# Optimization experiments

Measured on AMD Instinct MI355X. Metric: run time of the kernel, lower is better.

The kernel has to match this reference:

```python
import jax, jax.numpy as jnp
import numpy as np

N = 50000        # number of nodes (A is [N, N] sparse adjacency)
NNZ = 1600000    # number of edges (avg degree 32)
UNITS = 64       # output feature dim


def setup_inputs() -> dict:
    key = jax.random.key(0)
    k1, k2, k3, k4 = jax.random.split(key, 4)
    rows = jax.random.randint(k1, (NNZ,), 0, N, dtype=jnp.int32)
    cols = jax.random.randint(k2, (NNZ,), 0, N, dtype=jnp.int32)
    values = jax.random.uniform(k3, (NNZ,), dtype=jnp.float32)
    # glorot-like scale for kernel of shape (N, UNITS)
    kernel = jax.random.normal(k4, (N, UNITS), dtype=jnp.float32) * np.float32(1.0 / np.sqrt(N))
    bias = jnp.zeros((UNITS,), dtype=jnp.float32)
    return {"rows": rows, "cols": cols, "values": values, "kernel": kernel, "bias": bias}


def reference(rows, cols, values, kernel, bias):
    # Faithful math of: relu(dense(A) @ kernel + bias), computed as SpMM
    # (zeros of the densified A contribute nothing, so results are identical).
    gathered = values[:, None] * kernel[cols]           # [nnz, units]
    out = jax.ops.segment_sum(gathered, rows, num_segments=N)  # [N, units]
    return jax.nn.relu(out + bias)
```

## Files before the change

kernel.cpp:

```cpp
#include <hip/hip_runtime.h>

#define UNITS 64
#define NNODES 50000
#define NBUCK 512
#define CAP 3584
#define BIN_TPB 512
#define BIN_EPT 8
#define SPMM_TPB 1024

typedef unsigned long long u64;
typedef unsigned int u32;
typedef unsigned short u16;


__device__ __forceinline__ int rowbase_of(u32 b) {
    return (int)((b * 50000u + 511u) >> 9);
}

__global__ void gc_prep(const float* __restrict__ kf, u16* __restrict__ kb,
                        int* __restrict__ gcursor, int n4) {
    int i = blockIdx.x * blockDim.x + threadIdx.x;
    if (blockIdx.x == 0 && threadIdx.x < 256) {
        gcursor[threadIdx.x]       = threadIdx.x * CAP;
        gcursor[threadIdx.x + 256] = (threadIdx.x + 256) * CAP;
    }
    if (i >= n4) return;
    float4 f = ((const float4*)kf)[i];
    ushort4 o;
    u32 b;
    b = __float_as_uint(f.x); o.x = (u16)((b + 0x7FFFu + ((b >> 16) & 1u)) >> 16);
    b = __float_as_uint(f.y); o.y = (u16)((b + 0x7FFFu + ((b >> 16) & 1u)) >> 16);
    b = __float_as_uint(f.z); o.z = (u16)((b + 0x7FFFu + ((b >> 16) & 1u)) >> 16);
    b = __float_as_uint(f.w); o.w = (u16)((b + 0x7FFFu + ((b >> 16) & 1u)) >> 16);
    ((ushort4*)kb)[i] = o;
}

__global__ __launch_bounds__(BIN_TPB) void gc_bin(const int* __restrict__ rows,
                                                  const int* __restrict__ cols,
                                                  const float* __restrict__ values,
                                                  int* __restrict__ gcursor,
                                                  u64* __restrict__ edges, int nnz) {
    __shared__ u64 stage[BIN_TPB * BIN_EPT];
    __shared__ int hist[NBUCK];
    __shared__ int lstart[NBUCK];
    __shared__ int delta[NBUCK];
    int t = threadIdx.x;
    if (t < NBUCK) hist[t] = 0;
    __syncthreads();

    int blockStart = blockIdx.x * (BIN_TPB * BIN_EPT);
    int cnt = min(BIN_TPB * BIN_EPT, nnz - blockStart);

    u64 rec[BIN_EPT];
    int bk[BIN_EPT];
    int rk[BIN_EPT];
#pragma unroll
    for (int k = 0; k < BIN_EPT; ++k) {
        int idx = blockStart + k * BIN_TPB + t;
        if (idx < nnz) {
            int r = rows[idx];
            u32 c = (u32)cols[idx];
            u32 v = __float_as_uint(values[idx]);
            int b = (int)(((u32)r * 512u) / 50000u);
            int lrow = r - rowbase_of((u32)b);
            rec[k] = ((u64)v << 32) | ((u64)(u32)b << 23) | ((u64)(u32)lrow << 16) | (u64)c;
            bk[k] = b;
            rk[k] = atomicAdd(&hist[b], 1);
        } else {
            bk[k] = -1;
        }
    }
    __syncthreads();

    int v0 = (t < NBUCK) ? hist[t] : 0;
    lstart[t] = v0;
    __syncthreads();
    for (int off = 1; off < NBUCK; off <<= 1) {
        int x = (t >= off) ? lstart[t - off] : 0;
        __syncthreads();
        lstart[t] += x;
        __syncthreads();
    }
    {
        int excl = lstart[t] - v0;
        int gbase = (v0 > 0) ? atomicAdd(&gcursor[t], v0) : 0;
        delta[t] = gbase - excl;
        lstart[t] = excl;
    }
    __syncthreads();

#pragma unroll
    for (int k = 0; k < BIN_EPT; ++k) {
        if (bk[k] >= 0) stage[lstart[bk[k]] + rk[k]] = rec[k];
    }
    __syncthreads();

    for (int i = t; i < cnt; i += BIN_TPB) {
        u64 r = stage[i];
        int b = (int)((r >> 23) & 0x1FF);
        int gpos = delta[b] + i;
        if (gpos < (b + 1) * CAP) edges[gpos] = r;
    }
}

__global__ __launch_bounds__(SPMM_TPB) void gc_spmm(const u64* __restrict__ edges,
                                                    const int* __restrict__ gcursor,
                                                    const u16* __restrict__ kb,
                                                    const float* __restrict__ bias,
                                                    float* __restrict__ out) {
    __shared__ u64 stage[CAP];
    __shared__ int rhist[128];
    __shared__ int rstart[128];
    int b = blockIdx.x;
    int t = threadIdx.x;
    int rowlo = rowbase_of((u32)b);
    int nrows = rowbase_of((u32)b + 1u) - rowlo;
    int count = min(gcursor[b] - b * CAP, CAP);
    const u64* eb = edges + (size_t)b * CAP;

    if (t < 128) rhist[t] = 0;
    __syncthreads();

    u64 rec[4];
    int rk[4], lr[4];
#pragma unroll
    for (int k = 0; k < 4; ++k) {
        int i = k * SPMM_TPB + t;
        if (i < count) {
            u64 r = eb[i];
            rec[k] = r;
            int l = (int)((r >> 16) & 0x7F);
            lr[k] = l;
            rk[k] = atomicAdd(&rhist[l], 1);
        } else {
            lr[k] = -1;
        }
    }
    __syncthreads();

    int v0 = (t < 128) ? rhist[t] : 0;
    if (t < 128) rstart[t] = v0;
    __syncthreads();
    for (int off = 1; off < 128; off <<= 1) {
        int x = 0;
        if (t < 128 && t >= off) x = rstart[t - off];
        __syncthreads();
        if (t < 128) rstart[t] += x;
        __syncthreads();
    }
    if (t < 128) rstart[t] -= v0;
    __syncthreads();

#pragma unroll
    for (int k = 0; k < 4; ++k) {
        if (lr[k] >= 0) stage[rstart[lr[k]] + rk[k]] = rec[k];
    }
    __syncthreads();

    int lane = t & 63;
    int w = t >> 6;
    float bl = bias[lane];
    for (int row = w; row < nrows; row += 16) {
        int j = rstart[row];
        int e = rstart[row + 1];
        float acc = 0.0f;
        for (; j + 4 <= e; j += 4) {
            u64 r0 = stage[j + 0], r1 = stage[j + 1], r2 = stage[j + 2], r3 = stage[j + 3];
            float k0 = __uint_as_float((u32)kb[((u32)r0 & 0xFFFFu) * UNITS + lane] << 16);
            float k1 = __uint_as_float((u32)kb[((u32)r1 & 0xFFFFu) * UNITS + lane] << 16);
            float k2 = __uint_as_float((u32)kb[((u32)r2 & 0xFFFFu) * UNITS + lane] << 16);
            float k3 = __uint_as_float((u32)kb[((u32)r3 & 0xFFFFu) * UNITS + lane] << 16);
            acc = fmaf(__uint_as_float((u32)(r0 >> 32)), k0, acc);
            acc = fmaf(__uint_as_float((u32)(r1 >> 32)), k1, acc);
            acc = fmaf(__uint_as_float((u32)(r2 >> 32)), k2, acc);
            acc = fmaf(__uint_as_float((u32)(r3 >> 32)), k3, acc);
        }
        for (; j < e; ++j) {
            u64 r = stage[j];
            float k = __uint_as_float((u32)kb[((u32)r & 0xFFFFu) * UNITS + lane] << 16);
            acc = fmaf(__uint_as_float((u32)(r >> 32)), k, acc);
        }
        out[(size_t)(rowlo + row) * UNITS + lane] = fmaxf(acc + bl, 0.0f);
    }
}

extern "C" void kernel_launch(void* const* d_in, const int* in_sizes, int n_in,
                              void* d_out, int out_size, void* d_ws, size_t ws_size,
                              hipStream_t stream) {
    const int*   rows   = (const int*)d_in[0];
    const int*   cols   = (const int*)d_in[1];
    const float* values = (const float*)d_in[2];
    const float* kern   = (const float*)d_in[3];
    const float* bias   = (const float*)d_in[4];
    float* out = (float*)d_out;

    const int nnz = in_sizes[0];

    char* ws = (char*)d_ws;
    u16* kb      = (u16*)(ws + 0);
    int* gcursor = (int*)(ws + 6400000);
    u64* edges   = (u64*)(ws + 6402048);

    int n4 = (NNODES * UNITS) / 4;
    gc_prep<<<(n4 + 255) / 256, 256, 0, stream>>>(kern, kb, gcursor, n4);

    gc_bin<<<(nnz + BIN_TPB * BIN_EPT - 1) / (BIN_TPB * BIN_EPT), BIN_TPB, 0, stream>>>(
        rows, cols, values, gcursor, edges, nnz);

    gc_spmm<<<NBUCK, SPMM_TPB, 0, stream>>>(edges, gcursor, kb, bias, out);
}
```

Measured before the change: 135.1 us.

## Use wave-shuffle scans, double bin block size, and pair-edge SpMM gather

Replaces the shared-memory Hillis-Steele scans in both the binning and SpMM kernels with wave-level shuffle scans plus a small cross-wave fixup, cutting barrier counts. The binning block size goes from 512 to 1024 threads, so each block handles more edges and fewer blocks hit the global cursors. In the SpMM loop each wave now processes two edges at once, each half-wave loading 32-bit bf16 pairs, and the halves are combined with a shuffle before a float2 store. This trades more, narrower gathers for wider loads and fewer loop iterations, at the cost of one-iteration unrolling and predicated tails.

```diff
diff --git a/kernel.cpp b/kernel.cpp
--- a/kernel.cpp
+++ b/kernel.cpp
@@ -4,7 +4,7 @@
 #define NNODES 50000
 #define NBUCK 512
 #define CAP 3584
-#define BIN_TPB 512
+#define BIN_TPB 1024
 #define BIN_EPT 8
 #define SPMM_TPB 1024
 
@@ -44,6 +44,7 @@
     __shared__ int hist[NBUCK];
     __shared__ int lstart[NBUCK];
     __shared__ int delta[NBUCK];
+    __shared__ int wsum[8];
     int t = threadIdx.x;
     if (t < NBUCK) hist[t] = 0;
     __syncthreads();
@@ -72,20 +73,30 @@
     }
     __syncthreads();
 
-    int v0 = (t < NBUCK) ? hist[t] : 0;
-    lstart[t] = v0;
-    __syncthreads();
-    for (int off = 1; off < NBUCK; off <<= 1) {
-        int x = (t >= off) ? lstart[t - off] : 0;
-        __syncthreads();
-        lstart[t] += x;
-        __syncthreads();
-    }
     {
-        int excl = lstart[t] - v0;
-        int gbase = (v0 > 0) ? atomicAdd(&gcursor[t], v0) : 0;
-        delta[t] = gbase - excl;
-        lstart[t] = excl;
+        int wid = t >> 6, ln = t & 63;
+        int val = (t < NBUCK) ? hist[t] : 0;
+        if (wid < 8) {
+            for (int off = 1; off < 64; off <<= 1) {
+                int x = __shfl_up(val, off, 64);
+                if (ln >= off) val += x;
+            }
+            if (ln == 63) wsum[wid] = val;
+        }
+        __syncthreads();
+        if (t == 0) {
+            int s = 0;
+            for (int i = 0; i < 8; ++i) { int x = wsum[i]; wsum[i] = s; s += x; }
+        }
+        __syncthreads();
+        if (wid < 8) {
+            int incl = val + wsum[wid];
+            int excl = incl - hist[t];
+            int h = hist[t];
+            int gbase = (h > 0) ? atomicAdd(&gcursor[t], h) : 0;
+            delta[t] = gbase - excl;
+            lstart[t] = excl;
+        }
     }
     __syncthreads();
 
@@ -110,7 +121,8 @@
                                                     float* __restrict__ out) {
     __shared__ u64 stage[CAP];
     __shared__ int rhist[128];
-    __shared__ int rstart[128];
+    __shared__ int rstart[129];
+    __shared__ int wsum2[2];
     int b = blockIdx.x;
     int t = threadIdx.x;
     int rowlo = rowbase_of((u32)b);
@@ -138,17 +150,22 @@
     }
     __syncthreads();
 
-    int v0 = (t < 128) ? rhist[t] : 0;
-    if (t < 128) rstart[t] = v0;
-    __syncthreads();
-    for (int off = 1; off < 128; off <<= 1) {
-        int x = 0;
-        if (t < 128 && t >= off) x = rstart[t - off];
-        __syncthreads();
-        if (t < 128) rstart[t] += x;
-        __syncthreads();
-    }
-    if (t < 128) rstart[t] -= v0;
+    {
+        int wid = t >> 6, ln = t & 63;
+        int val = (t < 128) ? rhist[t] : 0;
+        if (wid < 2) {
+            for (int off = 1; off < 64; off <<= 1) {
+                int x = __shfl_up(val, off, 64);
+                if (ln >= off) val += x;
+            }
+            if (ln == 63) wsum2[wid] = val;
+        }
+        __syncthreads();
+        if (t == 0) { int a = wsum2[0]; wsum2[0] = 0; wsum2[1] = a; }
+        __syncthreads();
+        if (wid < 2) rstart[t] = val + wsum2[wid] - rhist[t];
+        if (t == 0) rstart[128] = count;
+    }
     __syncthreads();
 
 #pragma unroll
@@ -158,29 +175,37 @@
     __syncthreads();
 
     int lane = t & 63;
+    int half = lane >> 5;
+    int ul = lane & 31;
     int w = t >> 6;
-    float bl = bias[lane];
+    float2 bl = ((const float2*)bias)[ul];
+
     for (int row = w; row < nrows; row += 16) {
-        int j = rstart[row];
-        int e = rstart[row + 1];
-        float acc = 0.0f;
-        for (; j + 4 <= e; j += 4) {
-            u64 r0 = stage[j + 0], r1 = stage[j + 1], r2 = stage[j + 2], r3 = stage[j + 3];
-            float k0 = __uint_as_float((u32)kb[((u32)r0 & 0xFFFFu) * UNITS + lane] << 16);
-            float k1 = __uint_as_float((u32)kb[((u32)r1 & 0xFFFFu) * UNITS + lane] << 16);
-            float k2 = __uint_as_float((u32)kb[((u32)r2 & 0xFFFFu) * UNITS + lane] << 16);
-            float k3 = __uint_as_float((u32)kb[((u32)r3 & 0xFFFFu) * UNITS + lane] << 16);
-            acc = fmaf(__uint_as_float((u32)(r0 >> 32)), k0, acc);
-            acc = fmaf(__uint_as_float((u32)(r1 >> 32)), k1, acc);
-            acc = fmaf(__uint_as_float((u32)(r2 >> 32)), k2, acc);
-            acc = fmaf(__uint_as_float((u32)(r3 >> 32)), k3, acc);
-        }
-        for (; j < e; ++j) {
-            u64 r = stage[j];
-            float k = __uint_as_float((u32)kb[((u32)r & 0xFFFFu) * UNITS + lane] << 16);
-            acc = fmaf(__uint_as_float((u32)(r >> 32)), k, acc);
-        }
-        out[(size_t)(rowlo + row) * UNITS + lane] = fmaxf(acc + bl, 0.0f);
+        int j0 = rstart[row];
+        int e  = rstart[row + 1];
+        int npairs = (e - j0 + 1) >> 1;
+        float ax = 0.0f, ay = 0.0f;
+        for (int p = 0; p < npairs; ++p) {
+            int j = j0 + 2 * p + half;
+            float v = 0.0f, kx = 0.0f, ky = 0.0f;
+            if (j < e) {
+                u64 r = stage[j];
+                u32 kk = *(const u32*)(kb + ((u32)r & 0xFFFFu) * UNITS + 2 * ul);
+                kx = __uint_as_float(kk << 16);
+                ky = __uint_as_float(kk & 0xFFFF0000u);
+                v = __uint_as_float((u32)(r >> 32));
+            }
+            ax = fmaf(v, kx, ax);
+            ay = fmaf(v, ky, ay);
+        }
+        ax += __shfl_xor(ax, 32, 64);
+        ay += __shfl_xor(ay, 32, 64);
+        if (half == 0) {
+            float2 o;
+            o.x = fmaxf(ax + bl.x, 0.0f);
+            o.y = fmaxf(ay + bl.y, 0.0f);
+            ((float2*)out)[(size_t)(rowlo + row) * 32 + ul] = o;
+        }
     }
 }
 
```

Result: slower. 143.9 us (+6.5%).
